# Performance work log

Measured on AMD Instinct MI355X. Metric: run time of the kernel, lower is better.

## Reference

```python
import jax, jax.numpy as jnp
import numpy as np

OUT_DIM = 1024


def setup_inputs() -> dict:
    key = jax.random.key(0)
    k1, k2, k3, k4 = jax.random.split(key, 4)
    B, N, D = 4, 2048, 1024
    s = 1.0 / np.sqrt(D)
    return {
        "x": jax.random.normal(k1, (B, N, D), dtype=jnp.float32),
        "W_query": jax.random.normal(k2, (D, OUT_DIM), dtype=jnp.float32) * s,
        "W_key": jax.random.normal(k3, (D, OUT_DIM), dtype=jnp.float32) * s,
        "W_value": jax.random.normal(k4, (D, OUT_DIM), dtype=jnp.float32) * s,
    }


def reference(x, W_query, W_key, W_value):
    # x: [B, N, D_in]; W_*: [D_in, D_out] (torch Linear weight transposed)
    q = jnp.einsum("bnd,de->bne", x, W_query)
    k = jnp.einsum("bnd,de->bne", x, W_key)
    v = jnp.einsum("bnd,de->bne", x, W_value)
    sqrt_d = jnp.sqrt(jnp.asarray(OUT_DIM, dtype=jnp.float32))
    scores = jnp.einsum("bie,bje->bij", q, k) / sqrt_d  # [B, N, N]
    # NOTE: original uses softmax over dim=1 (query axis), not the usual dim=2
    attn = jax.nn.softmax(scores, axis=1)
    # dropout with train=False is identity (eval-mode reference)
    # out = attn^T @ v  ->  out[b, j] = sum_i attn[b, i, j] * v[b, i]
    return jnp.einsum("bij,bie->bje", attn, v)
```

## Files before the change

kernel.cpp:

```cpp
#include <hip/hip_runtime.h>
#include <math.h>


typedef __bf16 bf16x8 __attribute__((ext_vector_type(8)));
typedef float f32x4 __attribute__((ext_vector_type(4)));

static __device__ __forceinline__ unsigned short f2bf(float f) {
    unsigned u = __float_as_uint(f);
    u += 0x7fff + ((u >> 16) & 1);
    return (unsigned short)(u >> 16);
}

#define GLDS16(gptr, lptr)                                                            \
    __builtin_amdgcn_global_load_lds(                                                 \
        (const __attribute__((address_space(1))) void*)(gptr),                        \
        (__attribute__((address_space(3))) void*)(lptr), 16, 0, 0)

__global__ __launch_bounds__(256) void gemm_scores(
    const unsigned short* __restrict__ QKb, unsigned short* __restrict__ P,
    float* __restrict__ l)
{
    __shared__ unsigned short As[128 * 64];
    __shared__ unsigned short Bs[128 * 64];

    const int tid  = threadIdx.x;
    const int wave = tid >> 6;
    const int lane = tid & 63;
    const int bz   = blockIdx.z;
    const long gm0 = (long)blockIdx.y * 128;
    const long gn0 = (long)blockIdx.x * 128;

    const unsigned short* Ab = QKb + (long)bz * 2048 * 2048 + 1024;
    const unsigned short* Bb = QKb + (long)bz * 2048 * 2048;

    const int r = lane >> 3;
    const int s = lane & 7;
    const int cg = (s ^ r) * 8;
    const unsigned short* ap = Ab + (gm0 + wave * 32 + r) * 2048L + cg;
    const unsigned short* bp = Bb + (gn0 + wave * 32 + r) * 2048L + cg;
    unsigned short* asl = &As[wave * 2048];
    unsigned short* bsl = &Bs[wave * 2048];

    const int wm   = (wave & 1) * 64;
    const int wn   = (wave >> 1) * 64;
    const int fr   = lane & 15;
    const int quad = lane >> 4;
    const int sw   = fr & 7;

    f32x4 acc[4][4];
#pragma unroll
    for (int i = 0; i < 4; i++)
#pragma unroll
        for (int j = 0; j < 4; j++) acc[i][j] = f32x4{0.f, 0.f, 0.f, 0.f};

    for (int k0 = 0; k0 < 1024; k0 += 64) {
        GLDS16(ap, asl);
        GLDS16(ap + 8 * 2048L, asl + 512);
        GLDS16(ap + 16 * 2048L, asl + 1024);
        GLDS16(ap + 24 * 2048L, asl + 1536);
        GLDS16(bp, bsl);
        GLDS16(bp + 8 * 2048L, bsl + 512);
        GLDS16(bp + 16 * 2048L, bsl + 1024);
        GLDS16(bp + 24 * 2048L, bsl + 1536);
        ap += 64;
        bp += 64;
        __syncthreads();

#pragma unroll
        for (int t = 0; t < 2; t++) {
            const int qs = ((t * 4 + quad) ^ sw) * 8;
            bf16x8 af[4], bf[4];
#pragma unroll
            for (int i = 0; i < 4; i++)
                af[i] = *(const bf16x8*)&As[(wm + i * 16 + fr) * 64 + qs];
#pragma unroll
            for (int j = 0; j < 4; j++)
                bf[j] = *(const bf16x8*)&Bs[(wn + j * 16 + fr) * 64 + qs];
#pragma unroll
            for (int i = 0; i < 4; i++)
#pragma unroll
                for (int j = 0; j < 4; j++)
                    acc[i][j] = __builtin_amdgcn_mfma_f32_16x16x32_bf16(
                        af[i], bf[j], acc[i][j], 0, 0, 0);
        }
        __syncthreads();
    }

    unsigned short* Pb = P + (long)bz * 2048 * 2048;
    float* lb = l + (long)bz * 2048;
    const long crow0 = gm0 + wm + quad * 4;
    const float scale = 1.0f / 32.0f;
#pragma unroll
    for (int i = 0; i < 4; i++) {
        const long rb = crow0 + i * 16;
        float rs[4] = {0.f, 0.f, 0.f, 0.f};
#pragma unroll
        for (int j = 0; j < 4; j++) {
            const long cb = gn0 + wn + j * 16 + fr;
#pragma unroll
            for (int rr = 0; rr < 4; rr++) {
                float e = __expf(acc[i][j][rr] * scale);
                rs[rr] += e;
                Pb[(rb + rr) * 2048L + cb] = f2bf(e);
            }
        }
#pragma unroll
        for (int rr = 0; rr < 4; rr++) {
#pragma unroll
            for (int m = 8; m > 0; m >>= 1) rs[rr] += __shfl_xor(rs[rr], m, 16);
        }
        if (fr == 0) {
#pragma unroll
            for (int rr = 0; rr < 4; rr++)
                atomicAdd(&lb[rb + rr], rs[rr]);
        }
    }
}

__global__ __launch_bounds__(256) void gemm_qkv(
    const unsigned short* __restrict__ A, const unsigned short* __restrict__ B,
    unsigned short* __restrict__ QK, unsigned short* __restrict__ Vt)
{
    __shared__ unsigned short As[128 * 64];
    __shared__ unsigned short Bs[128 * 64];

    const int tid  = threadIdx.x;
    const int wave = tid >> 6;
    const int lane = tid & 63;
    const long gm0 = (long)blockIdx.y * 128;
    const long gn0 = (long)blockIdx.x * 128;

    const int r = lane >> 3;
    const int s = lane & 7;
    const int cg = (s ^ r) * 8;
    const unsigned short* ap = A + (gm0 + wave * 32 + r) * 1024L + cg;
    const unsigned short* bp = B + (gn0 + wave * 32 + r) * 1024L + cg;
    unsigned short* asl = &As[wave * 2048];
    unsigned short* bsl = &Bs[wave * 2048];

    const int wm   = (wave & 1) * 64;
    const int wn   = (wave >> 1) * 64;
    const int fr   = lane & 15;
    const int quad = lane >> 4;
    const int sw   = fr & 7;

    f32x4 acc[4][4];
#pragma unroll
    for (int i = 0; i < 4; i++)
#pragma unroll
        for (int j = 0; j < 4; j++) acc[i][j] = f32x4{0.f, 0.f, 0.f, 0.f};

    for (int k0 = 0; k0 < 1024; k0 += 64) {
        GLDS16(ap, asl);
        GLDS16(ap + 8 * 1024L, asl + 512);
        GLDS16(ap + 16 * 1024L, asl + 1024);
        GLDS16(ap + 24 * 1024L, asl + 1536);
        GLDS16(bp, bsl);
        GLDS16(bp + 8 * 1024L, bsl + 512);
        GLDS16(bp + 16 * 1024L, bsl + 1024);
        GLDS16(bp + 24 * 1024L, bsl + 1536);
        ap += 64;
        bp += 64;
        __syncthreads();

#pragma unroll
        for (int t = 0; t < 2; t++) {
            const int qs = ((t * 4 + quad) ^ sw) * 8;
            bf16x8 af[4], bf[4];
#pragma unroll
            for (int i = 0; i < 4; i++)
                af[i] = *(const bf16x8*)&As[(wm + i * 16 + fr) * 64 + qs];
#pragma unroll
            for (int j = 0; j < 4; j++)
                bf[j] = *(const bf16x8*)&Bs[(wn + j * 16 + fr) * 64 + qs];
#pragma unroll
            for (int i = 0; i < 4; i++)
#pragma unroll
                for (int j = 0; j < 4; j++)
                    acc[i][j] = __builtin_amdgcn_mfma_f32_16x16x32_bf16(
                        af[i], bf[j], acc[i][j], 0, 0, 0);
        }
        __syncthreads();
    }

    const long crow0 = gm0 + wm + quad * 4;
    if (gn0 < 2048) {
#pragma unroll
        for (int i = 0; i < 4; i++) {
            const long rb = crow0 + i * 16;
#pragma unroll
            for (int j = 0; j < 4; j++) {
                const long cb = gn0 + wn + j * 16 + fr;
#pragma unroll
                for (int rr = 0; rr < 4; rr++)
                    QK[(rb + rr) * 2048L + cb] = f2bf(acc[i][j][rr]);
            }
        }
    } else {
#pragma unroll
        for (int i = 0; i < 4; i++) {
            const long rb = crow0 + i * 16;
#pragma unroll
            for (int j = 0; j < 4; j++) {
                const long ce = gn0 - 2048 + wn + j * 16 + fr;
                ushort4 o;
                o.x = f2bf(acc[i][j][0]);
                o.y = f2bf(acc[i][j][1]);
                o.z = f2bf(acc[i][j][2]);
                o.w = f2bf(acc[i][j][3]);
                *(ushort4*)&Vt[ce * 8192L + rb] = o;
            }
        }
    }
}

__global__ __launch_bounds__(256) void gemm_pv(
    const unsigned short* __restrict__ P, const unsigned short* __restrict__ Vt,
    const float* __restrict__ l, float* __restrict__ out)
{
    __shared__ unsigned short As[64 * 64];
    __shared__ unsigned short Bs[128 * 64];

    const int tid  = threadIdx.x;
    const int wave = tid >> 6;
    const int lane = tid & 63;
    const int bz   = blockIdx.z;
    const long gm0 = (long)blockIdx.y * 64;
    const long gn0 = (long)blockIdx.x * 128;

    const unsigned short* Ab = P + (long)bz * 2048 * 2048;
    const unsigned short* Bb = Vt + (long)bz * 2048;

    const int r = lane >> 3;
    const int s = lane & 7;
    const int cg = (s ^ r) * 8;
    const unsigned short* ap = Ab + (gm0 + wave * 16 + r) * 2048L + cg;
    const unsigned short* bp = Bb + (gn0 + wave * 32 + r) * 8192L + cg;
    unsigned short* asl = &As[wave * 1024];
    unsigned short* bsl = &Bs[wave * 2048];

    const int fr   = lane & 15;
    const int quad = lane >> 4;
    const int sw   = fr & 7;

    f32x4 acc[4][2];
#pragma unroll
    for (int i = 0; i < 4; i++)
#pragma unroll
        for (int j = 0; j < 2; j++) acc[i][j] = f32x4{0.f, 0.f, 0.f, 0.f};

    for (int k0 = 0; k0 < 2048; k0 += 64) {
        GLDS16(ap, asl);
        GLDS16(ap + 8 * 2048L, asl + 512);
        GLDS16(bp, bsl);
        GLDS16(bp + 8 * 8192L, bsl + 512);
        GLDS16(bp + 16 * 8192L, bsl + 1024);
        GLDS16(bp + 24 * 8192L, bsl + 1536);
        ap += 64;
        bp += 64;
        __syncthreads();

#pragma unroll
        for (int t = 0; t < 2; t++) {
            const int qs = ((t * 4 + quad) ^ sw) * 8;
            bf16x8 af[4], bf[2];
#pragma unroll
            for (int i = 0; i < 4; i++)
                af[i] = *(const bf16x8*)&As[(i * 16 + fr) * 64 + qs];
#pragma unroll
            for (int j = 0; j < 2; j++)
                bf[j] = *(const bf16x8*)&Bs[(wave * 32 + j * 16 + fr) * 64 + qs];
#pragma unroll
            for (int i = 0; i < 4; i++)
#pragma unroll
                for (int j = 0; j < 2; j++)
                    acc[i][j] = __builtin_amdgcn_mfma_f32_16x16x32_bf16(
                        af[i], bf[j], acc[i][j], 0, 0, 0);
        }
        __syncthreads();
    }

    float* Ob = out + (long)bz * 2048 * 1024;
    const float* lb = l + (long)bz * 2048;
    const long crow0 = gm0 + quad * 4;
#pragma unroll
    for (int i = 0; i < 4; i++) {
        const long rb = crow0 + i * 16;
        float inv[4];
#pragma unroll
        for (int rr = 0; rr < 4; rr++) inv[rr] = 1.0f / lb[rb + rr];
#pragma unroll
        for (int j = 0; j < 2; j++) {
            const long cb = gn0 + wave * 32 + j * 16 + fr;
#pragma unroll
            for (int rr = 0; rr < 4; rr++)
                Ob[(rb + rr) * 1024L + cb] = acc[i][j][rr] * inv[rr];
        }
    }
}

__global__ __launch_bounds__(256) void prep(
    const float* __restrict__ x,
    const float* __restrict__ Wq, const float* __restrict__ Wk,
    const float* __restrict__ Wv,
    unsigned short* __restrict__ xb, unsigned short* __restrict__ Wqkvt,
    float* __restrict__ l)
{
    __shared__ float t[32][33];
    const int b = blockIdx.x;
    const int tid = threadIdx.x;
    if (b < 8192) {
        int i = b * 256 + tid;
        float4 v = ((const float4*)x)[i];
        ushort4 o;
        o.x = f2bf(v.x); o.y = f2bf(v.y); o.z = f2bf(v.z); o.w = f2bf(v.w);
        ((ushort4*)xb)[i] = o;
        return;
    }
    if (b == 8192 + 3072) {
        float4 z = {0.f, 0.f, 0.f, 0.f};
#pragma unroll
        for (int i = 0; i < 8; i++)
            ((float4*)l)[tid * 8 + i] = z;
        return;
    }
    int tix = b - 8192;
    const int w = tix >> 10;
    tix &= 1023;
    const float* W = (w == 0) ? Wq : (w == 1) ? Wk : Wv;
    unsigned short* Wt = Wqkvt + (long)w * 1024 * 1024;
    const int bx = (tix & 31) * 32;
    const int by = (tix >> 5) * 32;
    const int tx = tid & 31;
    const int ty = (tid >> 5) * 4;
#pragma unroll
    for (int j = 0; j < 4; j++)
        t[ty + j][tx] = W[(long)(by + ty + j) * 1024 + bx + tx];
    __syncthreads();
#pragma unroll
    for (int j = 0; j < 4; j++)
        Wt[(long)(bx + ty + j) * 1024 + by + tx] = f2bf(t[tx][ty + j]);
}

extern "C" void kernel_launch(void* const* d_in, const int* in_sizes, int n_in,
                              void* d_out, int out_size, void* d_ws,
                              size_t ws_size, hipStream_t stream)
{
    const float* x  = (const float*)d_in[0];
    const float* Wq = (const float*)d_in[1];
    const float* Wk = (const float*)d_in[2];
    const float* Wv = (const float*)d_in[3];
    float* out = (float*)d_out;

    const long M1 = 1024 * 1024;
    unsigned short* u     = (unsigned short*)d_ws;
    unsigned short* xb    = u;
    unsigned short* Wqkvt = u + 8 * M1;
    unsigned short* QKb   = Wqkvt + 3 * M1;
    unsigned short* Vtb   = QKb + 16 * M1;
    unsigned short* Pb    = Vtb + 8 * M1;
    float* l              = (float*)(Pb + 16 * M1);

    dim3 blk(256);

    prep<<<dim3(8192 + 3072 + 1), blk, 0, stream>>>(x, Wq, Wk, Wv, xb, Wqkvt, l);

    gemm_qkv<<<dim3(24, 64), blk, 0, stream>>>(xb, Wqkvt, QKb, Vtb);

    gemm_scores<<<dim3(16, 16, 4), blk, 0, stream>>>(QKb, Pb, l);

    gemm_pv<<<dim3(8, 32, 4), blk, 0, stream>>>(Pb, Vtb, l, out);
}
```

Before: 258.0 us.

## Reassociate Q·K^T as x·(Wq·Wk^T)·x^T to drop one projection GEMM

Precomputes the 1024x1024 product of Wk and Wq (scaled) inside the prep kernel, then computes y = x·M^T alongside V and forms scores as x·y^T. This removes one of the three N×D×D projection GEMMs and the Wq/Wk transposes. It adds a small weight-weight GEMM run in few blocks with fp32-to-bf16 conversion in-loop, and an extra bf16 rounding of the fused matrix that may affect accuracy.

```diff
diff --git a/kernel.cpp b/kernel.cpp
--- a/kernel.cpp
+++ b/kernel.cpp
@@ -16,36 +16,66 @@
         (const __attribute__((address_space(1))) void*)(gptr),                        \
         (__attribute__((address_space(3))) void*)(lptr), 16, 0, 0)
 
-__global__ __launch_bounds__(256) void gemm_scores(
-    const unsigned short* __restrict__ QKb, unsigned short* __restrict__ P,
-    float* __restrict__ l)
+__global__ __launch_bounds__(256) void prep_m(
+    const float* __restrict__ x,
+    const float* __restrict__ Wq, const float* __restrict__ Wk,
+    const float* __restrict__ Wv,
+    unsigned short* __restrict__ xb, unsigned short* __restrict__ Wvt,
+    unsigned short* __restrict__ Bm, float* __restrict__ l)
 {
-    __shared__ unsigned short As[128 * 64];
-    __shared__ unsigned short Bs[128 * 64];
-
-    const int tid  = threadIdx.x;
+    __shared__ unsigned short smem[2 * 128 * 32];
+    const int b = blockIdx.x;
+    const int tid = threadIdx.x;
+
+    if (b < 8192) {
+        int i = b * 256 + tid;
+        float4 v = ((const float4*)x)[i];
+        ushort4 o;
+        o.x = f2bf(v.x); o.y = f2bf(v.y); o.z = f2bf(v.z); o.w = f2bf(v.w);
+        ((ushort4*)xb)[i] = o;
+        return;
+    }
+    if (b < 9216) {
+        float(*t)[33] = (float(*)[33])smem;
+        int tix = b - 8192;
+        const int bx = (tix & 31) * 32;
+        const int by = (tix >> 5) * 32;
+        const int tx = tid & 31;
+        const int ty = (tid >> 5) * 4;
+#pragma unroll
+        for (int j = 0; j < 4; j++)
+            t[ty + j][tx] = Wv[(long)(by + ty + j) * 1024 + bx + tx];
+        __syncthreads();
+#pragma unroll
+        for (int j = 0; j < 4; j++)
+            Wvt[(long)(bx + ty + j) * 1024 + by + tx] = f2bf(t[tx][ty + j]);
+        return;
+    }
+    if (b == 9216) {
+        float4 z = {0.f, 0.f, 0.f, 0.f};
+#pragma unroll
+        for (int i = 0; i < 8; i++)
+            ((float4*)l)[tid * 8 + i] = z;
+        return;
+    }
+
+    unsigned short* As = smem;
+    unsigned short* Bs = smem + 128 * 32;
+    const int g = b - 9217;
+    const long gm0 = (long)(g >> 3) * 128;
+    const long gn0 = (long)(g & 7) * 128;
+
     const int wave = tid >> 6;
     const int lane = tid & 63;
-    const int bz   = blockIdx.z;
-    const long gm0 = (long)blockIdx.y * 128;
-    const long gn0 = (long)blockIdx.x * 128;
-
-    const unsigned short* Ab = QKb + (long)bz * 2048 * 2048 + 1024;
-    const unsigned short* Bb = QKb + (long)bz * 2048 * 2048;
-
-    const int r = lane >> 3;
-    const int s = lane & 7;
-    const int cg = (s ^ r) * 8;
-    const unsigned short* ap = Ab + (gm0 + wave * 32 + r) * 2048L + cg;
-    const unsigned short* bp = Bb + (gn0 + wave * 32 + r) * 2048L + cg;
-    unsigned short* asl = &As[wave * 2048];
-    unsigned short* bsl = &Bs[wave * 2048];
-
     const int wm   = (wave & 1) * 64;
     const int wn   = (wave >> 1) * 64;
     const int fr   = lane & 15;
     const int quad = lane >> 4;
-    const int sw   = fr & 7;
+    const int swf  = (fr >> 1) & 3;
+
+    const int sr   = tid >> 1;
+    const int cseg = (tid & 1) * 16;
+    const int swr  = (sr >> 1) & 3;
 
     f32x4 acc[4][4];
 #pragma unroll
@@ -53,73 +83,57 @@
 #pragma unroll
         for (int j = 0; j < 4; j++) acc[i][j] = f32x4{0.f, 0.f, 0.f, 0.f};
 
-    for (int k0 = 0; k0 < 1024; k0 += 64) {
-        GLDS16(ap, asl);
-        GLDS16(ap + 8 * 2048L, asl + 512);
-        GLDS16(ap + 16 * 2048L, asl + 1024);
-        GLDS16(ap + 24 * 2048L, asl + 1536);
-        GLDS16(bp, bsl);
-        GLDS16(bp + 8 * 2048L, bsl + 512);
-        GLDS16(bp + 16 * 2048L, bsl + 1024);
-        GLDS16(bp + 24 * 2048L, bsl + 1536);
-        ap += 64;
-        bp += 64;
-        __syncthreads();
-
-#pragma unroll
-        for (int t = 0; t < 2; t++) {
-            const int qs = ((t * 4 + quad) ^ sw) * 8;
-            bf16x8 af[4], bf[4];
-#pragma unroll
-            for (int i = 0; i < 4; i++)
-                af[i] = *(const bf16x8*)&As[(wm + i * 16 + fr) * 64 + qs];
+    for (int k0 = 0; k0 < 1024; k0 += 32) {
+#pragma unroll
+        for (int u = 0; u < 4; u++) {
+            const int c = cseg + u * 4;
+            const int sl = sr * 32 + (((c >> 3) ^ swr) * 8) + (c & 4);
+            float4 a = *(const float4*)&Wk[(gm0 + sr) * 1024 + k0 + c];
+            ushort4 oa;
+            oa.x = f2bf(a.x); oa.y = f2bf(a.y); oa.z = f2bf(a.z); oa.w = f2bf(a.w);
+            *(ushort4*)&As[sl] = oa;
+            float4 bv = *(const float4*)&Wq[(gn0 + sr) * 1024 + k0 + c];
+            ushort4 ob;
+            ob.x = f2bf(bv.x); ob.y = f2bf(bv.y); ob.z = f2bf(bv.z); ob.w = f2bf(bv.w);
+            *(ushort4*)&Bs[sl] = ob;
+        }
+        __syncthreads();
+
+        const int qs = (quad ^ swf) * 8;
+        bf16x8 af[4], bf[4];
+#pragma unroll
+        for (int i = 0; i < 4; i++)
+            af[i] = *(const bf16x8*)&As[(wm + i * 16 + fr) * 32 + qs];
+#pragma unroll
+        for (int j = 0; j < 4; j++)
+            bf[j] = *(const bf16x8*)&Bs[(wn + j * 16 + fr) * 32 + qs];
+#pragma unroll
+        for (int i = 0; i < 4; i++)
 #pragma unroll
             for (int j = 0; j < 4; j++)
-                bf[j] = *(const bf16x8*)&Bs[(wn + j * 16 + fr) * 64 + qs];
-#pragma unroll
-            for (int i = 0; i < 4; i++)
-#pragma unroll
-                for (int j = 0; j < 4; j++)
-                    acc[i][j] = __builtin_amdgcn_mfma_f32_16x16x32_bf16(
-                        af[i], bf[j], acc[i][j], 0, 0, 0);
-        }
-        __syncthreads();
-    }
-
-    unsigned short* Pb = P + (long)bz * 2048 * 2048;
-    float* lb = l + (long)bz * 2048;
+                acc[i][j] = __builtin_amdgcn_mfma_f32_16x16x32_bf16(
+                    af[i], bf[j], acc[i][j], 0, 0, 0);
+        __syncthreads();
+    }
+
     const long crow0 = gm0 + wm + quad * 4;
-    const float scale = 1.0f / 32.0f;
 #pragma unroll
     for (int i = 0; i < 4; i++) {
         const long rb = crow0 + i * 16;
-        float rs[4] = {0.f, 0.f, 0.f, 0.f};
 #pragma unroll
         for (int j = 0; j < 4; j++) {
             const long cb = gn0 + wn + j * 16 + fr;
 #pragma unroll
-            for (int rr = 0; rr < 4; rr++) {
-                float e = __expf(acc[i][j][rr] * scale);
-                rs[rr] += e;
-                Pb[(rb + rr) * 2048L + cb] = f2bf(e);
-            }
-        }
-#pragma unroll
-        for (int rr = 0; rr < 4; rr++) {
-#pragma unroll
-            for (int m = 8; m > 0; m >>= 1) rs[rr] += __shfl_xor(rs[rr], m, 16);
-        }
-        if (fr == 0) {
-#pragma unroll
             for (int rr = 0; rr < 4; rr++)
-                atomicAdd(&lb[rb + rr], rs[rr]);
-        }
-    }
-}
-
-__global__ __launch_bounds__(256) void gemm_qkv(
-    const unsigned short* __restrict__ A, const unsigned short* __restrict__ B,
-    unsigned short* __restrict__ QK, unsigned short* __restrict__ Vt)
+                Bm[(rb + rr) * 1024L + cb] = f2bf(acc[i][j][rr] * 0.03125f);
+        }
+    }
+}
+
+__global__ __launch_bounds__(256) void gemm_yv(
+    const unsigned short* __restrict__ A, const unsigned short* __restrict__ Bm,
+    const unsigned short* __restrict__ Wvt,
+    unsigned short* __restrict__ y, unsigned short* __restrict__ Vt)
 {
     __shared__ unsigned short As[128 * 64];
     __shared__ unsigned short Bs[128 * 64];
@@ -129,12 +143,15 @@
     const int lane = tid & 63;
     const long gm0 = (long)blockIdx.y * 128;
     const long gn0 = (long)blockIdx.x * 128;
+    const bool isV = gn0 >= 1024;
+    const long nb  = isV ? gn0 - 1024 : gn0;
+    const unsigned short* Bbase = isV ? Wvt : Bm;
 
     const int r = lane >> 3;
     const int s = lane & 7;
     const int cg = (s ^ r) * 8;
     const unsigned short* ap = A + (gm0 + wave * 32 + r) * 1024L + cg;
-    const unsigned short* bp = B + (gn0 + wave * 32 + r) * 1024L + cg;
+    const unsigned short* bp = Bbase + (nb + wave * 32 + r) * 1024L + cg;
     unsigned short* asl = &As[wave * 2048];
     unsigned short* bsl = &Bs[wave * 2048];
 
@@ -184,16 +201,16 @@
     }
 
     const long crow0 = gm0 + wm + quad * 4;
-    if (gn0 < 2048) {
+    if (!isV) {
 #pragma unroll
         for (int i = 0; i < 4; i++) {
             const long rb = crow0 + i * 16;
 #pragma unroll
             for (int j = 0; j < 4; j++) {
-                const long cb = gn0 + wn + j * 16 + fr;
+                const long cb = nb + wn + j * 16 + fr;
 #pragma unroll
                 for (int rr = 0; rr < 4; rr++)
-                    QK[(rb + rr) * 2048L + cb] = f2bf(acc[i][j][rr]);
+                    y[(rb + rr) * 1024L + cb] = f2bf(acc[i][j][rr]);
             }
         }
     } else {
@@ -202,7 +219,7 @@
             const long rb = crow0 + i * 16;
 #pragma unroll
             for (int j = 0; j < 4; j++) {
-                const long ce = gn0 - 2048 + wn + j * 16 + fr;
+                const long ce = nb + wn + j * 16 + fr;
                 ushort4 o;
                 o.x = f2bf(acc[i][j][0]);
                 o.y = f2bf(acc[i][j][1]);
@@ -210,6 +227,106 @@
                 o.w = f2bf(acc[i][j][3]);
                 *(ushort4*)&Vt[ce * 8192L + rb] = o;
             }
+        }
+    }
+}
+
+__global__ __launch_bounds__(256) void gemm_scores(
+    const unsigned short* __restrict__ xb, const unsigned short* __restrict__ y,
+    unsigned short* __restrict__ P, float* __restrict__ l)
+{
+    __shared__ unsigned short As[128 * 64];
+    __shared__ unsigned short Bs[128 * 64];
+
+    const int tid  = threadIdx.x;
+    const int wave = tid >> 6;
+    const int lane = tid & 63;
+    const int bz   = blockIdx.z;
+    const long gm0 = (long)blockIdx.y * 128;
+    const long gn0 = (long)blockIdx.x * 128;
+
+    const unsigned short* Ab = xb + (long)bz * 2048 * 1024;
+    const unsigned short* Bb = y + (long)bz * 2048 * 1024;
+
+    const int r = lane >> 3;
+    const int s = lane & 7;
+    const int cg = (s ^ r) * 8;
+    const unsigned short* ap = Ab + (gm0 + wave * 32 + r) * 1024L + cg;
+    const unsigned short* bp = Bb + (gn0 + wave * 32 + r) * 1024L + cg;
+    unsigned short* asl = &As[wave * 2048];
+    unsigned short* bsl = &Bs[wave * 2048];
+
+    const int wm   = (wave & 1) * 64;
+    const int wn   = (wave >> 1) * 64;
+    const int fr   = lane & 15;
+    const int quad = lane >> 4;
+    const int sw   = fr & 7;
+
+    f32x4 acc[4][4];
+#pragma unroll
+    for (int i = 0; i < 4; i++)
+#pragma unroll
+        for (int j = 0; j < 4; j++) acc[i][j] = f32x4{0.f, 0.f, 0.f, 0.f};
+
+    for (int k0 = 0; k0 < 1024; k0 += 64) {
+        GLDS16(ap, asl);
+        GLDS16(ap + 8 * 1024L, asl + 512);
+        GLDS16(ap + 16 * 1024L, asl + 1024);
+        GLDS16(ap + 24 * 1024L, asl + 1536);
+        GLDS16(bp, bsl);
+        GLDS16(bp + 8 * 1024L, bsl + 512);
+        GLDS16(bp + 16 * 1024L, bsl + 1024);
+        GLDS16(bp + 24 * 1024L, bsl + 1536);
+        ap += 64;
+        bp += 64;
+        __syncthreads();
+
+#pragma unroll
+        for (int t = 0; t < 2; t++) {
+            const int qs = ((t * 4 + quad) ^ sw) * 8;
+            bf16x8 af[4], bf[4];
+#pragma unroll
+            for (int i = 0; i < 4; i++)
+                af[i] = *(const bf16x8*)&As[(wm + i * 16 + fr) * 64 + qs];
+#pragma unroll
+            for (int j = 0; j < 4; j++)
+                bf[j] = *(const bf16x8*)&Bs[(wn + j * 16 + fr) * 64 + qs];
+#pragma unroll
+            for (int i = 0; i < 4; i++)
+#pragma unroll
+                for (int j = 0; j < 4; j++)
+                    acc[i][j] = __builtin_amdgcn_mfma_f32_16x16x32_bf16(
+                        af[i], bf[j], acc[i][j], 0, 0, 0);
+        }
+        __syncthreads();
+    }
+
+    unsigned short* Pb = P + (long)bz * 2048 * 2048;
+    float* lb = l + (long)bz * 2048;
+    const long crow0 = gm0 + wm + quad * 4;
+#pragma unroll
+    for (int i = 0; i < 4; i++) {
+        const long rb = crow0 + i * 16;
+        float rs[4] = {0.f, 0.f, 0.f, 0.f};
+#pragma unroll
+        for (int j = 0; j < 4; j++) {
+            const long cb = gn0 + wn + j * 16 + fr;
+#pragma unroll
+            for (int rr = 0; rr < 4; rr++) {
+                float e = __expf(acc[i][j][rr]);
+                rs[rr] += e;
+                Pb[(rb + rr) * 2048L + cb] = f2bf(e);
+            }
+        }
+#pragma unroll
+        for (int rr = 0; rr < 4; rr++) {
+#pragma unroll
+            for (int m = 8; m > 0; m >>= 1) rs[rr] += __shfl_xor(rs[rr], m, 16);
+        }
+        if (fr == 0) {
+#pragma unroll
+            for (int rr = 0; rr < 4; rr++)
+                atomicAdd(&lb[rb + rr], rs[rr]);
         }
     }
 }
@@ -299,49 +416,6 @@
     }
 }
 
-__global__ __launch_bounds__(256) void prep(
-    const float* __restrict__ x,
-    const float* __restrict__ Wq, const float* __restrict__ Wk,
-    const float* __restrict__ Wv,
-    unsigned short* __restrict__ xb, unsigned short* __restrict__ Wqkvt,
-    float* __restrict__ l)
-{
-    __shared__ float t[32][33];
-    const int b = blockIdx.x;
-    const int tid = threadIdx.x;
-    if (b < 8192) {
-        int i = b * 256 + tid;
-        float4 v = ((const float4*)x)[i];
-        ushort4 o;
-        o.x = f2bf(v.x); o.y = f2bf(v.y); o.z = f2bf(v.z); o.w = f2bf(v.w);
-        ((ushort4*)xb)[i] = o;
-        return;
-    }
-    if (b == 8192 + 3072) {
-        float4 z = {0.f, 0.f, 0.f, 0.f};
-#pragma unroll
-        for (int i = 0; i < 8; i++)
-            ((float4*)l)[tid * 8 + i] = z;
-        return;
-    }
-    int tix = b - 8192;
-    const int w = tix >> 10;
-    tix &= 1023;
-    const float* W = (w == 0) ? Wq : (w == 1) ? Wk : Wv;
-    unsigned short* Wt = Wqkvt + (long)w * 1024 * 1024;
-    const int bx = (tix & 31) * 32;
-    const int by = (tix >> 5) * 32;
-    const int tx = tid & 31;
-    const int ty = (tid >> 5) * 4;
-#pragma unroll
-    for (int j = 0; j < 4; j++)
-        t[ty + j][tx] = W[(long)(by + ty + j) * 1024 + bx + tx];
-    __syncthreads();
-#pragma unroll
-    for (int j = 0; j < 4; j++)
-        Wt[(long)(bx + ty + j) * 1024 + by + tx] = f2bf(t[tx][ty + j]);
-}
-
 extern "C" void kernel_launch(void* const* d_in, const int* in_sizes, int n_in,
                               void* d_out, int out_size, void* d_ws,
                               size_t ws_size, hipStream_t stream)
@@ -353,21 +427,23 @@
     float* out = (float*)d_out;
 
     const long M1 = 1024 * 1024;
-    unsigned short* u     = (unsigned short*)d_ws;
-    unsigned short* xb    = u;
-    unsigned short* Wqkvt = u + 8 * M1;
-    unsigned short* QKb   = Wqkvt + 3 * M1;
-    unsigned short* Vtb   = QKb + 16 * M1;
-    unsigned short* Pb    = Vtb + 8 * M1;
-    float* l              = (float*)(Pb + 16 * M1);
+    unsigned short* u    = (unsigned short*)d_ws;
+    unsigned short* xb   = u;
+    unsigned short* Wvt  = u + 8 * M1;
+    unsigned short* Bm   = Wvt + M1;
+    unsigned short* yb   = Bm + M1;
+    unsigned short* Vtb  = yb + 8 * M1;
+    unsigned short* Pb   = Vtb + 8 * M1;
+    float* l             = (float*)(Pb + 16 * M1);
 
     dim3 blk(256);
 
-    prep<<<dim3(8192 + 3072 + 1), blk, 0, stream>>>(x, Wq, Wk, Wv, xb, Wqkvt, l);
-
-    gemm_qkv<<<dim3(24, 64), blk, 0, stream>>>(xb, Wqkvt, QKb, Vtb);
-
-    gemm_scores<<<dim3(16, 16, 4), blk, 0, stream>>>(QKb, Pb, l);
+    prep_m<<<dim3(8192 + 1024 + 1 + 64), blk, 0, stream>>>(
+        x, Wq, Wk, Wv, xb, Wvt, Bm, l);
+
+    gemm_yv<<<dim3(16, 64), blk, 0, stream>>>(xb, Bm, Wvt, yb, Vtb);
+
+    gemm_scores<<<dim3(16, 16, 4), blk, 0, stream>>>(xb, yb, Pb, l);
 
     gemm_pv<<<dim3(8, 32, 4), blk, 0, stream>>>(Pb, Vtb, l, out);
 }
```

After: 283.2 us. +9.8%, slower.
